# Kernel optimization log

Hardware: AMD Instinct MI355X
Metric: run time of the kernel (lower is better)

The kernel has to match this reference:

```python
import math
import jax, jax.numpy as jnp
import numpy as np

B, L, D_MODEL = 2, 2048, 768
H = 12            # num_heads == num_key_value_heads
FEAT = 16         # feature_dim
HEAD_DIM = D_MODEL // H  # 64


def taylor_exp(x):
    """Taylor-exp feature map: phi(x) = [1, x/rrd, (x (x) x)/(sqrt(2)*rd)].
    x: [..., d] -> [..., 1 + d + d^2]"""
    d = x.shape[-1]
    rd = math.sqrt(d)
    rrd = math.sqrt(rd)
    r2 = math.sqrt(2.0)
    x2 = (x[..., :, None] * x[..., None, :]).reshape(*x.shape[:-1], d * d) / r2
    ones = jnp.ones(x.shape[:-1] + (1,), dtype=x.dtype)
    return jnp.concatenate([ones, x / rrd, x2 / rd], axis=-1)


def setup_inputs() -> dict:
    key = jax.random.key(0)
    k1, k2, k3, k4, k5 = jax.random.split(key, 5)
    s = 0.02
    return {
        "hidden_states": jax.random.normal(k1, (B, L, D_MODEL), jnp.float32),
        "Wq": jax.random.normal(k2, (H * FEAT, D_MODEL), jnp.float32) * s,
        "Wk": jax.random.normal(k3, (H * FEAT, D_MODEL), jnp.float32) * s,
        "Wv": jax.random.normal(k4, (D_MODEL, D_MODEL), jnp.float32) * s,
        "Wo": jax.random.normal(k5, (D_MODEL, D_MODEL), jnp.float32) * s,
    }


def reference(hidden_states, Wq, Wk, Wv, Wo):
    b, l, d = hidden_states.shape
    # projections (torch Linear, no bias): y = x @ W.T
    q = jnp.einsum('bld,fd->blf', hidden_states, Wq).reshape(b, l, H, FEAT).transpose(0, 2, 1, 3)
    k = jnp.einsum('bld,fd->blf', hidden_states, Wk).reshape(b, l, H, FEAT).transpose(0, 2, 1, 3)
    v = jnp.einsum('bld,fd->blf', hidden_states, Wv).reshape(b, l, H, HEAD_DIM).transpose(0, 2, 1, 3)

    q = taylor_exp(q)   # [b,h,l,Dexp]
    k = taylor_exp(k)   # k_enc == k (forward clones k), v_enc == v

    # denominator: k_enc.sum over seq + causal cumsum of k
    k_state = jnp.sum(k, axis=2, keepdims=True) + jnp.cumsum(k, axis=2)  # [b,h,l,Dexp]
    z = 1.0 / jnp.sum(q * k_state, axis=-1)                              # [b,h,l]

    # quadratic scores; y1 uses causal (tril) mask, y2 uses full scores with same k,v
    A = jnp.einsum('bhnd,bhmd->bhnm', q, k)                              # [b,h,l,l]
    causal = jnp.tril(jnp.ones((l, l), dtype=A.dtype))
    A_total = A * causal + A                                             # tril(A) + A
    y = jnp.einsum('bhnm,bhme->bhne', A_total, v) * z[..., None]         # [b,h,l,e]

    out = y.transpose(0, 2, 1, 3).reshape(b, l, H * HEAD_DIM)
    return jnp.einsum('blf,df->bld', out, Wo)
```

## Files before the change

### kernel.cpp

```cpp
#include <hip/hip_runtime.h>

typedef unsigned short ushortT;
typedef __bf16 bf16x8 __attribute__((ext_vector_type(8)));
typedef float f32x4 __attribute__((ext_vector_type(4)));

#define BB   2
#define LL   2048
#define DM   768
#define HH   12
#define FT   16
#define HD   64
#define DEXP 273
#define CH   128
#define NC   16
#define NBH  24
#define NBLK 384
#define C2f  0.17677669529663687f
#define KH   768
#define KP   1536

__device__ __forceinline__ void split_bf16(float x, ushortT& hi, ushortT& lo) {
  unsigned b = __float_as_uint(x);
  unsigned r = b + 0x7FFFu + ((b >> 16) & 1u);
  hi = (ushortT)(r >> 16);
  float hf = __uint_as_float((unsigned)hi << 16);
  lo = (ushortT)(__float_as_uint(x - hf) >> 16);
}

__global__ __launch_bounds__(256) void pack_a(const float* __restrict__ X,
                                              ushortT* __restrict__ Xh,
                                              int total4) {
  int g = blockIdx.x * 256 + threadIdx.x;
  if (g >= total4) return;
  int m = g / 192, k4 = (g % 192) * 4;
  float4 v = *(const float4*)(X + (size_t)m * 768 + k4);
  ushortT h[4], l[4];
  split_bf16(v.x, h[0], l[0]);
  split_bf16(v.y, h[1], l[1]);
  split_bf16(v.z, h[2], l[2]);
  split_bf16(v.w, h[3], l[3]);
  ushortT* p = Xh + (size_t)m * KP + k4;
  *(ushort4*)p = *(ushort4*)h;
  *(ushort4*)(p + KH) = *(ushort4*)l;
}

__global__ __launch_bounds__(256) void pack_w(const float* __restrict__ W0,
                                              const float* __restrict__ W1,
                                              const float* __restrict__ W2,
                                              int n1, int n2,
                                              ushortT* __restrict__ Wh,
                                              int total4) {
  int g = blockIdx.x * 256 + threadIdx.x;
  if (g >= total4) return;
  int n = g / 192, k4 = (g % 192) * 4;
  const float* src = (n < n1 ? W0 + (size_t)n * 768
                    : n < n2 ? W1 + (size_t)(n - n1) * 768
                             : W2 + (size_t)(n - n2) * 768);
  float4 v = *(const float4*)(src + k4);
  ushortT h[4], l[4];
  split_bf16(v.x, h[0], l[0]);
  split_bf16(v.y, h[1], l[1]);
  split_bf16(v.z, h[2], l[2]);
  split_bf16(v.w, h[3], l[3]);
  ushortT* p = Wh + (size_t)n * KP + k4;
  *(ushort4*)p = *(ushort4*)h;
  *(ushort4*)(p + KH) = *(ushort4*)l;
}

typedef const __attribute__((address_space(1))) unsigned gq_t;
typedef __attribute__((address_space(3))) unsigned lq_t;
__device__ __forceinline__ void gload_lds16(const ushortT* g, ushortT* l) {
  __builtin_amdgcn_global_load_lds((gq_t*)g, (lq_t*)l, 16, 0, 0);
}

__global__ __launch_bounds__(256) void mfma_gemm(const ushortT* __restrict__ A,
                                                 const ushortT* __restrict__ B,
                                                 float* __restrict__ Y, int ldy,
                                                 int ntiles) {
  __shared__ ushortT sAh[128 * 32], sAl[128 * 32], sBh[64 * 32], sBl[64 * 32];
  const int blk = blockIdx.x;
  const int xcd = blk & 7, slot = blk >> 3;
  const int mtp = gridDim.x / (8 * ntiles);
  const int mt = xcd * mtp + slot / ntiles;
  const int nt = slot % ntiles;
  const int bm = mt * 128, bn = nt * 64;
  const int tid = threadIdx.x, wave = tid >> 6, lane = tid & 63;
  const int srow = lane >> 2, schk = (lane & 3) * 8;
  const ushortT* gsrc;
  ushortT* lb;
  int iters;
  switch (wave) {
    case 0:  gsrc = A + (size_t)(bm + srow) * KP + schk;      lb = sAh; iters = 8; break;
    case 1:  gsrc = A + (size_t)(bm + srow) * KP + KH + schk; lb = sAl; iters = 8; break;
    case 2:  gsrc = B + (size_t)(bn + srow) * KP + schk;      lb = sBh; iters = 4; break;
    default: gsrc = B + (size_t)(bn + srow) * KP + KH + schk; lb = sBl; iters = 4; break;
  }
  const int wm = (wave & 1) * 64, wn = (wave >> 1) * 32;
  const int fr = lane & 15, quad = lane >> 4;
  f32x4 acc[4][2] = {};
  for (int k0 = 0; k0 < KH; k0 += 32) {
    __syncthreads();
    for (int it = 0; it < iters; it++)
      gload_lds16(gsrc + k0 + (size_t)it * 16 * KP, lb + it * 512);
    __syncthreads();
    bf16x8 ah[4], al[4], bh2[2], bl2[2];
#pragma unroll
    for (int mi = 0; mi < 4; mi++) {
      ah[mi] = *(const bf16x8*)&sAh[(wm + mi * 16 + fr) * 32 + quad * 8];
      al[mi] = *(const bf16x8*)&sAl[(wm + mi * 16 + fr) * 32 + quad * 8];
    }
#pragma unroll
    for (int ni = 0; ni < 2; ni++) {
      bh2[ni] = *(const bf16x8*)&sBh[(wn + ni * 16 + fr) * 32 + quad * 8];
      bl2[ni] = *(const bf16x8*)&sBl[(wn + ni * 16 + fr) * 32 + quad * 8];
    }
#pragma unroll
    for (int mi = 0; mi < 4; mi++)
#pragma unroll
      for (int ni = 0; ni < 2; ni++) {
        acc[mi][ni] = __builtin_amdgcn_mfma_f32_16x16x32_bf16(ah[mi], bh2[ni], acc[mi][ni], 0, 0, 0);
        acc[mi][ni] = __builtin_amdgcn_mfma_f32_16x16x32_bf16(ah[mi], bl2[ni], acc[mi][ni], 0, 0, 0);
        acc[mi][ni] = __builtin_amdgcn_mfma_f32_16x16x32_bf16(al[mi], bh2[ni], acc[mi][ni], 0, 0, 0);
      }
  }
  const int orow = quad * 4;
#pragma unroll
  for (int mi = 0; mi < 4; mi++)
#pragma unroll
    for (int ni = 0; ni < 2; ni++) {
      float* yp = Y + (size_t)(bm + wm + mi * 16 + orow) * ldy + bn + wn + ni * 16 + fr;
#pragma unroll
      for (int r = 0; r < 4; r++) yp[(size_t)r * ldy] = acc[mi][ni][r];
    }
}

__global__ __launch_bounds__(256, 2) void chunk_sum_kernel(
    const float* __restrict__ qkv, float* __restrict__ csS,
    float* __restrict__ csk) {
  const int blk = blockIdx.x;
  const int bh = blk >> 4, c = blk & 15;
  const int b = bh / HH, h = bh % HH;
  __shared__ float kT[16][128];
  __shared__ ushortT phiA[288][72];
  __shared__ ushortT Vt[64][72];
  const float* base = qkv + (size_t)(b * LL + c * CH) * 1152;
  const int tid = threadIdx.x;
  const int wave = tid >> 6, lane = tid & 63;
  const int fr = lane & 15, quad = lane >> 4;
  for (int idx = tid; idx < 512; idx += 256) {
    int m = idx >> 2, i4 = (idx & 3) * 4;
    float4 k4 = *(const float4*)&base[(size_t)m * 1152 + 192 + h * 16 + i4];
    kT[i4 + 0][m] = k4.x; kT[i4 + 1][m] = k4.y;
    kT[i4 + 2][m] = k4.z; kT[i4 + 3][m] = k4.w;
  }
  const int wm2 = (wave & 1) * 144, wn2 = (wave >> 1) * 32;
  f32x4 acc[9][2] = {};
  __syncthreads();
#pragma unroll 1
  for (int s = 0; s < 4; s++) {
    const int m0 = s * 32;
    if (s) __syncthreads();
    for (int idx = tid; idx < 512; idx += 256) {
      int m = m0 + (idx >> 4), e4 = (idx & 15) * 4;
      float4 v4 = *(const float4*)&base[(size_t)m * 1152 + 384 + h * 64 + e4];
      ushortT hh[4], ll[4];
      split_bf16(v4.x, hh[0], ll[0]); split_bf16(v4.y, hh[1], ll[1]);
      split_bf16(v4.z, hh[2], ll[2]); split_bf16(v4.w, hh[3], ll[3]);
      const int mi2 = m - m0;
#pragma unroll
      for (int j = 0; j < 4; j++) {
        Vt[e4 + j][mi2] = hh[j];
        Vt[e4 + j][32 + mi2] = ll[j];
      }
    }
    for (int rr = tid; rr < 288; rr += 256) {
      const int f = rr;
      const float* pa = (f >= 17) ? kT[(f - 17) >> 4] : (f >= 1 ? kT[f - 1] : kT[0]);
      const float* pb = (f >= 17) ? kT[(f - 17) & 15] : kT[0];
      const float sc = (f == 0) ? 1.0f : (f < 17 ? 0.5f : C2f);
      const bool quadf = (f >= 17);
      const bool valid = (f < DEXP);
      ushortT hrow[32], lrow[32];
#pragma unroll
      for (int g = 0; g < 8; g++) {
        float4 a4 = *(const float4*)&pa[m0 + g * 4];
        float4 b4 = *(const float4*)&pb[m0 + g * 4];
        float v0, v1, v2, v3;
        if (f == 0) {
          v0 = v1 = v2 = v3 = 1.0f;
        } else if (!quadf) {
          v0 = sc * a4.x; v1 = sc * a4.y; v2 = sc * a4.z; v3 = sc * a4.w;
        } else {
          v0 = sc * a4.x * b4.x; v1 = sc * a4.y * b4.y;
          v2 = sc * a4.z * b4.z; v3 = sc * a4.w * b4.w;
        }
        if (!valid) { v0 = v1 = v2 = v3 = 0.0f; }
        split_bf16(v0, hrow[g * 4 + 0], lrow[g * 4 + 0]);
        split_bf16(v1, hrow[g * 4 + 1], lrow[g * 4 + 1]);
        split_bf16(v2, hrow[g * 4 + 2], lrow[g * 4 + 2]);
        split_bf16(v3, hrow[g * 4 + 3], lrow[g * 4 + 3]);
      }
      *(uint4*)&phiA[f][0] = *(uint4*)&hrow[0];
      *(uint4*)&phiA[f][8] = *(uint4*)&hrow[8];
      *(uint4*)&phiA[f][16] = *(uint4*)&hrow[16];
      *(uint4*)&phiA[f][24] = *(uint4*)&hrow[24];
      *(uint4*)&phiA[f][32] = *(uint4*)&lrow[0];
      *(uint4*)&phiA[f][40] = *(uint4*)&lrow[8];
      *(uint4*)&phiA[f][48] = *(uint4*)&lrow[16];
      *(uint4*)&phiA[f][56] = *(uint4*)&lrow[24];
    }
    __syncthreads();
    bf16x8 bhf[2], blf[2];
#pragma unroll
    for (int ni = 0; ni < 2; ni++) {
      bhf[ni] = *(const bf16x8*)&Vt[wn2 + ni * 16 + fr][quad * 8];
      blf[ni] = *(const bf16x8*)&Vt[wn2 + ni * 16 + fr][32 + quad * 8];
    }
#pragma unroll
    for (int mi = 0; mi < 9; mi++) {
      bf16x8 ah = *(const bf16x8*)&phiA[wm2 + mi * 16 + fr][quad * 8];
      bf16x8 al = *(const bf16x8*)&phiA[wm2 + mi * 16 + fr][32 + quad * 8];
#pragma unroll
      for (int ni = 0; ni < 2; ni++) {
        acc[mi][ni] = __builtin_amdgcn_mfma_f32_16x16x32_bf16(ah, bhf[ni], acc[mi][ni], 0, 0, 0);
        acc[mi][ni] = __builtin_amdgcn_mfma_f32_16x16x32_bf16(ah, blf[ni], acc[mi][ni], 0, 0, 0);
        acc[mi][ni] = __builtin_amdgcn_mfma_f32_16x16x32_bf16(al, bhf[ni], acc[mi][ni], 0, 0, 0);
      }
    }
  }
  for (int f = tid; f < DEXP; f += 256) {
    float sum = 0.0f;
    if (f == 0) {
      sum = (float)CH;
    } else if (f < 17) {
      const float* p = kT[f - 1];
      for (int m = 0; m < CH; m += 4) {
        float4 x = *(const float4*)&p[m];
        sum += x.x + x.y + x.z + x.w;
      }
      sum *= 0.5f;
    } else {
      const float* pa2 = kT[(f - 17) >> 4];
      const float* pb2 = kT[(f - 17) & 15];
      for (int m = 0; m < CH; m += 4) {
        float4 x = *(const float4*)&pa2[m];
        float4 y = *(const float4*)&pb2[m];
        sum += x.x * y.x + x.y * y.y + x.z * y.z + x.w * y.w;
      }
      sum *= C2f;
    }
    csk[(size_t)blk * DEXP + f] = sum;
  }
  float* S = csS + (size_t)blk * DEXP * 64;
#pragma unroll
  for (int mi = 0; mi < 9; mi++)
#pragma unroll
    for (int ni = 0; ni < 2; ni++)
#pragma unroll
      for (int r = 0; r < 4; r++) {
        const int f = wm2 + mi * 16 + quad * 4 + r;
        if (f < DEXP) S[(size_t)f * 64 + wn2 + ni * 16 + fr] = acc[mi][ni][r];
      }
}

__global__ __launch_bounds__(256) void prefix_kernel(float* __restrict__ csS,
                                                     float* __restrict__ csk) {
  const int gid = blockIdx.x * 256 + threadIdx.x;
  const int totS = NBH * DEXP * 64;
  if (gid < totS) {
    const int bh = gid / (DEXP * 64);
    const int idx = gid % (DEXP * 64);
    float r[NC];
    float tot = 0.0f;
#pragma unroll
    for (int c = 0; c < NC; c++) {
      r[c] = csS[(size_t)(bh * NC + c) * DEXP * 64 + idx];
      tot += r[c];
    }
    float run = 0.0f;
#pragma unroll
    for (int c = 0; c < NC; c++) {
      csS[(size_t)(bh * NC + c) * DEXP * 64 + idx] = run + tot;
      run += r[c];
    }
  } else {
    const int g2 = gid - totS;
    if (g2 < NBH * DEXP) {
      const int bh = g2 / DEXP;
      const int f = g2 % DEXP;
      float r[NC];
      float tot = 0.0f;
#pragma unroll
      for (int c = 0; c < NC; c++) {
        r[c] = csk[(size_t)(bh * NC + c) * DEXP + f];
        tot += r[c];
      }
      float run = 0.0f;
#pragma unroll
      for (int c = 0; c < NC; c++) {
        csk[(size_t)(bh * NC + c) * DEXP + f] = run + tot;
        run += r[c];
      }
    }
  }
}

__global__ __launch_bounds__(256, 2) void state_kernel(
    const float* __restrict__ qkv, const float* __restrict__ csS,
    float* __restrict__ att) {
  const int blk = blockIdx.x;
  const int bh = blk >> 4, c = blk & 15;
  const int b = bh / HH, h = bh % HH;
  __shared__ ushortT phiA[2][128][72];
  __shared__ ushortT Gt[2][64][72];
  const int tid = threadIdx.x;
  const int wv = tid >> 6, lane = tid & 63;
  const int prow = tid >> 1, phalf = tid & 1;
  const float* qrow = qkv + (size_t)(b * LL + c * CH + prow) * 1152 + h * 16;
  float qr[16];
#pragma unroll
  for (int i = 0; i < 4; i++) {
    float4 v = *(const float4*)(qrow + i * 4);
    qr[i * 4 + 0] = v.x; qr[i * 4 + 1] = v.y;
    qr[i * 4 + 2] = v.z; qr[i * 4 + 3] = v.w;
  }
  const float* Gc = csS + (size_t)blk * DEXP * 64;
  const int gfi = tid >> 4, gn4 = (tid & 15) * 4;

#define STAGE_SLAB(S, BB)                                                     \
  {                                                                           \
    const int f0 = (S) * 32;                                                  \
    _Pragma("unroll")                                                         \
    for (int p = 0; p < 2; p++) {                                             \
      const int fi = gfi + p * 16;                                            \
      const int f = f0 + fi;                                                  \
      float4 g = make_float4(0.f, 0.f, 0.f, 0.f);                             \
      if (f < DEXP) g = *(const float4*)(Gc + (size_t)f * 64 + gn4);          \
      ushortT gh[4], gl[4];                                                   \
      split_bf16(g.x, gh[0], gl[0]);                                          \
      split_bf16(g.y, gh[1], gl[1]);                                          \
      split_bf16(g.z, gh[2], gl[2]);                                          \
      split_bf16(g.w, gh[3], gl[3]);                                          \
      _Pragma("unroll")                                                       \
      for (int j = 0; j < 4; j++) {                                           \
        Gt[BB][gn4 + j][fi] = gh[j];                                          \
        Gt[BB][gn4 + j][32 + fi] = gl[j];                                     \
      }                                                                       \
    }                                                                         \
    ushortT h16[16], l16[16];                                                 \
    _Pragma("unroll")                                                         \
    for (int j = 0; j < 16; j++) {                                            \
      const int f = f0 + phalf * 16 + j;                                      \
      float v;                                                                \
      if (f == 0) v = 1.0f;                                                   \
      else if (f < 17) v = 0.5f * qr[f - 1];                                  \
      else if (f < DEXP) {                                                    \
        int ii = f - 17;                                                      \
        v = C2f * qr[ii >> 4] * qr[ii & 15];                                  \
      } else v = 0.0f;                                                        \
      split_bf16(v, h16[j], l16[j]);                                          \
    }                                                                         \
    *(uint4*)&phiA[BB][prow][phalf * 16] = *(uint4*)&h16[0];                  \
    *(uint4*)&phiA[BB][prow][phalf * 16 + 8] = *(uint4*)&h16[8];              \
    *(uint4*)&phiA[BB][prow][32 + phalf * 16] = *(uint4*)&l16[0];             \
    *(uint4*)&phiA[BB][prow][32 + phalf * 16 + 8] = *(uint4*)&l16[8];         \
  }

  const int fr = lane & 15, quad = lane >> 4;
  f32x4 acc[2][4] = {};
  STAGE_SLAB(0, 0);
  __syncthreads();
#pragma unroll 1
  for (int s = 0; s < 9; s++) {
    if (s < 8) STAGE_SLAB(s + 1, (s + 1) & 1);
    const int bb = s & 1;
    bf16x8 ah[2], al[2];
#pragma unroll
    for (int mi = 0; mi < 2; mi++) {
      ah[mi] = *(const bf16x8*)&phiA[bb][wv * 32 + mi * 16 + fr][quad * 8];
      al[mi] = *(const bf16x8*)&phiA[bb][wv * 32 + mi * 16 + fr][32 + quad * 8];
    }
#pragma unroll
    for (int ni = 0; ni < 4; ni++) {
      bf16x8 bh2 = *(const bf16x8*)&Gt[bb][ni * 16 + fr][quad * 8];
      bf16x8 bl2 = *(const bf16x8*)&Gt[bb][ni * 16 + fr][32 + quad * 8];
#pragma unroll
      for (int mi = 0; mi < 2; mi++) {
        acc[mi][ni] = __builtin_amdgcn_mfma_f32_16x16x32_bf16(ah[mi], bh2, acc[mi][ni], 0, 0, 0);
        acc[mi][ni] = __builtin_amdgcn_mfma_f32_16x16x32_bf16(ah[mi], bl2, acc[mi][ni], 0, 0, 0);
        acc[mi][ni] = __builtin_amdgcn_mfma_f32_16x16x32_bf16(al[mi], bh2, acc[mi][ni], 0, 0, 0);
      }
    }
    __syncthreads();
  }
  const int orow = quad * 4;
#pragma unroll
  for (int mi = 0; mi < 2; mi++)
#pragma unroll
    for (int ni = 0; ni < 4; ni++) {
      float* yp = att + (size_t)(b * LL + c * CH + wv * 32 + mi * 16 + orow) * DM +
                  h * 64 + ni * 16 + fr;
#pragma unroll
      for (int r = 0; r < 4; r++) yp[(size_t)r * DM] = acc[mi][ni][r];
    }
#undef STAGE_SLAB
}

__global__ __launch_bounds__(256) void intra_kernel(
    const float* __restrict__ qkv, const float* __restrict__ csk,
    float* __restrict__ att) {
  const int blk = blockIdx.x, tt = blockIdx.y;
  const int bh = blk >> 4, c = blk & 15;
  const int b = bh / HH, h = bh % HH;
  const int t0 = tt * 32, Mn = t0 + 32;
  __shared__ float ks[CH][17];
  __shared__ float vs[CH][68];
  __shared__ float qst[32][17];
  __shared__ float a_s[32][132];
  __shared__ float gkl[DEXP];
  __shared__ float dred[32][9];
  __shared__ float zl[32];
  const float* base = qkv + (size_t)(b * LL + c * CH) * 1152;
  const int tid = threadIdx.x;
  for (int idx = tid; idx < Mn * 16; idx += 256) {
    int m = idx >> 4, i = idx & 15;
    ks[m][i] = base[(size_t)m * 1152 + 192 + h * 16 + i];
  }
  for (int idx = tid; idx < Mn * 16; idx += 256) {
    int m = idx >> 4, e4g = (idx & 15) * 4;
    *(float4*)&vs[m][e4g] = *(const float4*)&base[(size_t)m * 1152 + 384 + h * 64 + e4g];
  }
  for (int idx = tid; idx < 32 * 16; idx += 256) {
    int t = idx >> 4, i = idx & 15;
    qst[t][i] = base[(size_t)(t0 + t) * 1152 + h * 16 + i];
  }
  for (int f = tid; f < DEXP; f += 256) gkl[f] = csk[(size_t)blk * DEXP + f];
  __syncthreads();
  for (int idx = tid; idx < 32 * CH; idx += 256) {
    const int t = idx >> 7, m = idx & 127;
    if (m < Mn) {
      float s = 0.0f;
#pragma unroll
      for (int i = 0; i < 16; i++) s += qst[t][i] * ks[m][i];
      a_s[t][m] = (m <= t0 + t) ? fmaf(s, fmaf(s, 0.03125f, 0.25f), 1.0f) : 0.0f;
    }
  }
  {
    const int t = tid >> 3, p = tid & 7;
    float part = (p == 0) ? gkl[0] : 0.0f;
#pragma unroll
    for (int ii = 0; ii < 2; ii++) {
      const int i = p * 2 + ii;
      const float qi = qst[t][i];
      part += 0.5f * qi * gkl[1 + i];
      float qsum = 0.0f;
#pragma unroll
      for (int j = 0; j < 16; j++) qsum += qst[t][j] * gkl[17 + i * 16 + j];
      part += C2f * qi * qsum;
    }
    dred[t][p] = part;
  }
  __syncthreads();
  if (tid < 32) {
    float dsum = 0.0f;
    for (int m = 0; m < Mn; m++) dsum += a_s[tid][m];
    float dstt = 0.0f;
#pragma unroll
    for (int p = 0; p < 8; p++) dstt += dred[tid][p];
    zl[tid] = 1.0f / (dstt + dsum);
  }
  __syncthreads();
  const int e4 = (tid & 15) * 4, tq = tid >> 4;
  float ac0[4] = {0, 0, 0, 0}, ac1[4] = {0, 0, 0, 0};
  for (int m = 0; m < Mn; m++) {
    float v4[4];
    *(float4*)v4 = *(const float4*)&vs[m][e4];
    const float a0 = a_s[tq][m], a1 = a_s[tq + 16][m];
#pragma unroll
    for (int j = 0; j < 4; j++) { ac0[j] += a0 * v4[j]; ac1[j] += a1 * v4[j]; }
  }
  const float z0 = zl[tq], z1 = zl[tq + 16];
  float* o0 = att + (size_t)(b * LL + c * CH + t0 + tq) * DM + h * 64 + e4;
  float* o1 = att + (size_t)(b * LL + c * CH + t0 + tq + 16) * DM + h * 64 + e4;
  float4 y0 = *(const float4*)o0;
  float4 y1 = *(const float4*)o1;
  float4 w0, w1;
  w0.x = (y0.x + ac0[0]) * z0; w0.y = (y0.y + ac0[1]) * z0;
  w0.z = (y0.z + ac0[2]) * z0; w0.w = (y0.w + ac0[3]) * z0;
  w1.x = (y1.x + ac1[0]) * z1; w1.y = (y1.y + ac1[1]) * z1;
  w1.z = (y1.z + ac1[2]) * z1; w1.w = (y1.w + ac1[3]) * z1;
  *(float4*)o0 = w0;
  *(float4*)o1 = w1;
}

extern "C" void kernel_launch(void* const* d_in, const int* in_sizes, int n_in,
                              void* d_out, int out_size, void* d_ws, size_t ws_size,
                              hipStream_t stream) {
  const float* hs = (const float*)d_in[0];
  const float* Wq = (const float*)d_in[1];
  const float* Wk = (const float*)d_in[2];
  const float* Wv = (const float*)d_in[3];
  const float* Wo = (const float*)d_in[4];
  float* out = (float*)d_out;
  char* ws = (char*)d_ws;
  float* qkv = (float*)(ws);
  float* att = (float*)(ws + 18874368);
  char*  regR = ws + 31457280;
  float* csS = (float*)regR;
  float* csk = (float*)(ws + 58294272);
  ushortT* Xhat = (ushortT*)regR;
  ushortT* What = (ushortT*)att;
  ushortT* Wohat = (ushortT*)qkv;
  ushortT* Ahat = (ushortT*)regR;
  const dim3 thr(256);
  pack_a<<<3072, thr, 0, stream>>>(hs, Xhat, 4096 * 192);
  pack_w<<<864, thr, 0, stream>>>(Wq, Wk, Wv, 192, 384, What, 1152 * 192);
  mfma_gemm<<<576, thr, 0, stream>>>(Xhat, What, qkv, 1152, 18);
  chunk_sum_kernel<<<NBLK, thr, 0, stream>>>(qkv, csS, csk);
  {
    const int tot = NBH * DEXP * 64 + NBH * DEXP;
    prefix_kernel<<<(tot + 255) / 256, thr, 0, stream>>>(csS, csk);
  }
  state_kernel<<<NBLK, thr, 0, stream>>>(qkv, csS, att);
  intra_kernel<<<dim3(NBLK, 4), thr, 0, stream>>>(qkv, csk, att);
  pack_w<<<576, thr, 0, stream>>>(Wo, Wo, Wo, 768, 768, Wohat, 768 * 192);
  pack_a<<<3072, thr, 0, stream>>>(att, Ahat, 4096 * 192);
  mfma_gemm<<<384, thr, 0, stream>>>(Ahat, Wohat, out, DM, 12);
}
```

Baseline: 273.5 us.

## Fuse state, intra-chunk attention and A packing into one MFMA kernel

Merges the inter-chunk state kernel, the intra-chunk scalar attention kernel and the pack_a of the attention output into a single kernel. The intra-chunk q·k scores and the P·V product now run on split-bf16 MFMA, and the row-sum denominator comes from an extra ones column. Normalised output is written straight in the hi/lo packed layout the output GEMM expects. This removes two launches, the att round trip through global memory and the scalar intra loop. In exchange the double buffering in the state loop is dropped, and the extra shared memory and registers may lower occupancy.

```diff
diff --git a/kernel.cpp b/kernel.cpp
--- a/kernel.cpp
+++ b/kernel.cpp
@@ -305,18 +305,26 @@
   }
 }
 
-__global__ __launch_bounds__(256, 2) void state_kernel(
+__global__ __launch_bounds__(256, 2) void fused_out(
     const float* __restrict__ qkv, const float* __restrict__ csS,
-    float* __restrict__ att) {
+    const float* __restrict__ csk, ushortT* __restrict__ Ahat) {
   const int blk = blockIdx.x;
   const int bh = blk >> 4, c = blk & 15;
   const int b = bh / HH, h = bh % HH;
-  __shared__ ushortT phiA[2][128][72];
-  __shared__ ushortT Gt[2][64][72];
+  __shared__ ushortT phiA[128][72];
+  __shared__ ushortT Gt[64][72];
+  __shared__ ushortT qA1[128][40];
+  __shared__ ushortT qA2[128][40];
+  __shared__ ushortT kB[32][40];
+  __shared__ ushortT onesB[16][72];
+  __shared__ float dred[128][2];
+  __shared__ float zl[128];
   const int tid = threadIdx.x;
   const int wv = tid >> 6, lane = tid & 63;
+  const int fr = lane & 15, quad = lane >> 4;
   const int prow = tid >> 1, phalf = tid & 1;
-  const float* qrow = qkv + (size_t)(b * LL + c * CH + prow) * 1152 + h * 16;
+  const float* base = qkv + (size_t)(b * LL + c * CH) * 1152;
+  const float* qrow = base + (size_t)prow * 1152 + h * 16;
   float qr[16];
 #pragma unroll
   for (int i = 0; i < 4; i++) {
@@ -324,66 +332,75 @@
     qr[i * 4 + 0] = v.x; qr[i * 4 + 1] = v.y;
     qr[i * 4 + 2] = v.z; qr[i * 4 + 3] = v.w;
   }
+  {
+    ushortT qh[16], ql[16];
+#pragma unroll
+    for (int i = 0; i < 16; i++) split_bf16(qr[i], qh[i], ql[i]);
+    *(uint4*)&qA1[prow][phalf * 16] = *(uint4*)&qh[0];
+    *(uint4*)&qA1[prow][phalf * 16 + 8] = *(uint4*)&qh[8];
+    *(uint4*)&qA2[prow][phalf * 16] = *(uint4*)&ql[0];
+    *(uint4*)&qA2[prow][phalf * 16 + 8] = *(uint4*)&ql[8];
+  }
+  for (int idx = tid; idx < 16 * 64; idx += 256) {
+    int row = idx >> 6, k = idx & 63;
+    onesB[row][k] = (row == 0 && k < 32) ? (ushortT)0x3F80 : (ushortT)0;
+  }
   const float* Gc = csS + (size_t)blk * DEXP * 64;
+  const float* gkp = csk + (size_t)blk * DEXP;
   const int gfi = tid >> 4, gn4 = (tid & 15) * 4;
-
-#define STAGE_SLAB(S, BB)                                                     \
-  {                                                                           \
-    const int f0 = (S) * 32;                                                  \
-    _Pragma("unroll")                                                         \
-    for (int p = 0; p < 2; p++) {                                             \
-      const int fi = gfi + p * 16;                                            \
-      const int f = f0 + fi;                                                  \
-      float4 g = make_float4(0.f, 0.f, 0.f, 0.f);                             \
-      if (f < DEXP) g = *(const float4*)(Gc + (size_t)f * 64 + gn4);          \
-      ushortT gh[4], gl[4];                                                   \
-      split_bf16(g.x, gh[0], gl[0]);                                          \
-      split_bf16(g.y, gh[1], gl[1]);                                          \
-      split_bf16(g.z, gh[2], gl[2]);                                          \
-      split_bf16(g.w, gh[3], gl[3]);                                          \
-      _Pragma("unroll")                                                       \
-      for (int j = 0; j < 4; j++) {                                           \
-        Gt[BB][gn4 + j][fi] = gh[j];                                          \
-        Gt[BB][gn4 + j][32 + fi] = gl[j];                                     \
-      }                                                                       \
-    }                                                                         \
-    ushortT h16[16], l16[16];                                                 \
-    _Pragma("unroll")                                                         \
-    for (int j = 0; j < 16; j++) {                                            \
-      const int f = f0 + phalf * 16 + j;                                      \
-      float v;                                                                \
-      if (f == 0) v = 1.0f;                                                   \
-      else if (f < 17) v = 0.5f * qr[f - 1];                                  \
-      else if (f < DEXP) {                                                    \
-        int ii = f - 17;                                                      \
-        v = C2f * qr[ii >> 4] * qr[ii & 15];                                  \
-      } else v = 0.0f;                                                        \
-      split_bf16(v, h16[j], l16[j]);                                          \
-    }                                                                         \
-    *(uint4*)&phiA[BB][prow][phalf * 16] = *(uint4*)&h16[0];                  \
-    *(uint4*)&phiA[BB][prow][phalf * 16 + 8] = *(uint4*)&h16[8];              \
-    *(uint4*)&phiA[BB][prow][32 + phalf * 16] = *(uint4*)&l16[0];             \
-    *(uint4*)&phiA[BB][prow][32 + phalf * 16 + 8] = *(uint4*)&l16[8];         \
-  }
-
-  const int fr = lane & 15, quad = lane >> 4;
-  f32x4 acc[2][4] = {};
-  STAGE_SLAB(0, 0);
-  __syncthreads();
+  f32x4 acc[2][5] = {};
+  float dacc = 0.0f;
 #pragma unroll 1
   for (int s = 0; s < 9; s++) {
-    if (s < 8) STAGE_SLAB(s + 1, (s + 1) & 1);
-    const int bb = s & 1;
+    const int f0 = s * 32;
+#pragma unroll
+    for (int p = 0; p < 2; p++) {
+      const int fi = gfi + p * 16;
+      const int f = f0 + fi;
+      float4 g = make_float4(0.f, 0.f, 0.f, 0.f);
+      if (f < DEXP) g = *(const float4*)(Gc + (size_t)f * 64 + gn4);
+      ushortT gh[4], gl[4];
+      split_bf16(g.x, gh[0], gl[0]);
+      split_bf16(g.y, gh[1], gl[1]);
+      split_bf16(g.z, gh[2], gl[2]);
+      split_bf16(g.w, gh[3], gl[3]);
+#pragma unroll
+      for (int j = 0; j < 4; j++) {
+        Gt[gn4 + j][fi] = gh[j];
+        Gt[gn4 + j][32 + fi] = gl[j];
+      }
+    }
+    {
+      ushortT h16[16], l16[16];
+#pragma unroll
+      for (int j = 0; j < 16; j++) {
+        const int f = f0 + phalf * 16 + j;
+        float v;
+        if (f == 0) v = 1.0f;
+        else if (f < 17) v = 0.5f * qr[f - 1];
+        else if (f < DEXP) {
+          int ii = f - 17;
+          v = C2f * qr[ii >> 4] * qr[ii & 15];
+        } else v = 0.0f;
+        if (f < DEXP) dacc += v * gkp[f];
+        split_bf16(v, h16[j], l16[j]);
+      }
+      *(uint4*)&phiA[prow][phalf * 16] = *(uint4*)&h16[0];
+      *(uint4*)&phiA[prow][phalf * 16 + 8] = *(uint4*)&h16[8];
+      *(uint4*)&phiA[prow][32 + phalf * 16] = *(uint4*)&l16[0];
+      *(uint4*)&phiA[prow][32 + phalf * 16 + 8] = *(uint4*)&l16[8];
+    }
+    __syncthreads();
     bf16x8 ah[2], al[2];
 #pragma unroll
     for (int mi = 0; mi < 2; mi++) {
-      ah[mi] = *(const bf16x8*)&phiA[bb][wv * 32 + mi * 16 + fr][quad * 8];
-      al[mi] = *(const bf16x8*)&phiA[bb][wv * 32 + mi * 16 + fr][32 + quad * 8];
+      ah[mi] = *(const bf16x8*)&phiA[wv * 32 + mi * 16 + fr][quad * 8];
+      al[mi] = *(const bf16x8*)&phiA[wv * 32 + mi * 16 + fr][32 + quad * 8];
     }
 #pragma unroll
     for (int ni = 0; ni < 4; ni++) {
-      bf16x8 bh2 = *(const bf16x8*)&Gt[bb][ni * 16 + fr][quad * 8];
-      bf16x8 bl2 = *(const bf16x8*)&Gt[bb][ni * 16 + fr][32 + quad * 8];
+      bf16x8 bh2 = *(const bf16x8*)&Gt[ni * 16 + fr][quad * 8];
+      bf16x8 bl2 = *(const bf16x8*)&Gt[ni * 16 + fr][32 + quad * 8];
 #pragma unroll
       for (int mi = 0; mi < 2; mi++) {
         acc[mi][ni] = __builtin_amdgcn_mfma_f32_16x16x32_bf16(ah[mi], bh2, acc[mi][ni], 0, 0, 0);
@@ -393,104 +410,100 @@
     }
     __syncthreads();
   }
-  const int orow = quad * 4;
+  dred[prow][phalf] = dacc;
+#pragma unroll 1
+  for (int s = 0; s < 4; s++) {
+    const int m0 = s * 32;
+    for (int idx = tid; idx < 128; idx += 256) {
+      int mL = idx >> 2, i4 = (idx & 3) * 4;
+      float4 k4 = *(const float4*)&base[(size_t)(m0 + mL) * 1152 + 192 + h * 16 + i4];
+      ushortT hh[4], ll[4];
+      split_bf16(k4.x, hh[0], ll[0]); split_bf16(k4.y, hh[1], ll[1]);
+      split_bf16(k4.z, hh[2], ll[2]); split_bf16(k4.w, hh[3], ll[3]);
+      *(ushort4*)&kB[mL][i4] = *(ushort4*)hh;
+      *(ushort4*)&kB[mL][16 + i4] = *(ushort4*)ll;
+    }
+    for (int idx = tid; idx < 512; idx += 256) {
+      int mL = idx >> 4, e4 = (idx & 15) * 4;
+      float4 v4 = *(const float4*)&base[(size_t)(m0 + mL) * 1152 + 384 + h * 64 + e4];
+      ushortT hh[4], ll[4];
+      split_bf16(v4.x, hh[0], ll[0]); split_bf16(v4.y, hh[1], ll[1]);
+      split_bf16(v4.z, hh[2], ll[2]); split_bf16(v4.w, hh[3], ll[3]);
+#pragma unroll
+      for (int j = 0; j < 4; j++) {
+        Gt[e4 + j][mL] = hh[j];
+        Gt[e4 + j][32 + mL] = ll[j];
+      }
+    }
+    __syncthreads();
+    if (s <= wv) {
+#pragma unroll
+      for (int rt = 0; rt < 2; rt++) {
+        bf16x8 a1 = *(const bf16x8*)&qA1[wv * 32 + rt * 16 + fr][quad * 8];
+        bf16x8 a2 = *(const bf16x8*)&qA2[wv * 32 + rt * 16 + fr][quad * 8];
+#pragma unroll
+        for (int mtt = 0; mtt < 2; mtt++) {
+          bf16x8 bk = *(const bf16x8*)&kB[mtt * 16 + fr][quad * 8];
+          f32x4 sf = {};
+          sf = __builtin_amdgcn_mfma_f32_16x16x32_bf16(a1, bk, sf, 0, 0, 0);
+          sf = __builtin_amdgcn_mfma_f32_16x16x32_bf16(a2, bk, sf, 0, 0, 0);
+          const int mg = m0 + mtt * 16 + fr;
+#pragma unroll
+          for (int r = 0; r < 4; r++) {
+            const int rowL = wv * 32 + rt * 16 + quad * 4 + r;
+            const float sv = sf[r];
+            const float p = (mg <= rowL) ? fmaf(sv, fmaf(sv, 0.03125f, 0.25f), 1.0f) : 0.0f;
+            ushortT ph, pl;
+            split_bf16(p, ph, pl);
+            phiA[rowL][mtt * 16 + fr] = ph;
+            phiA[rowL][32 + mtt * 16 + fr] = pl;
+          }
+        }
+      }
+#pragma unroll
+      for (int mi = 0; mi < 2; mi++) {
+        bf16x8 ah = *(const bf16x8*)&phiA[wv * 32 + mi * 16 + fr][quad * 8];
+        bf16x8 al = *(const bf16x8*)&phiA[wv * 32 + mi * 16 + fr][32 + quad * 8];
+#pragma unroll
+        for (int ni = 0; ni < 5; ni++) {
+          bf16x8 bh2 = (ni < 4) ? *(const bf16x8*)&Gt[ni * 16 + fr][quad * 8]
+                                : *(const bf16x8*)&onesB[fr][quad * 8];
+          bf16x8 bl2 = (ni < 4) ? *(const bf16x8*)&Gt[ni * 16 + fr][32 + quad * 8]
+                                : *(const bf16x8*)&onesB[fr][32 + quad * 8];
+          acc[mi][ni] = __builtin_amdgcn_mfma_f32_16x16x32_bf16(ah, bh2, acc[mi][ni], 0, 0, 0);
+          acc[mi][ni] = __builtin_amdgcn_mfma_f32_16x16x32_bf16(ah, bl2, acc[mi][ni], 0, 0, 0);
+          acc[mi][ni] = __builtin_amdgcn_mfma_f32_16x16x32_bf16(al, bh2, acc[mi][ni], 0, 0, 0);
+        }
+      }
+    }
+    __syncthreads();
+  }
+  if (fr == 0) {
+#pragma unroll
+    for (int mi = 0; mi < 2; mi++)
+#pragma unroll
+      for (int r = 0; r < 4; r++) {
+        const int rowL = wv * 32 + mi * 16 + quad * 4 + r;
+        const float d = dred[rowL][0] + dred[rowL][1] + acc[mi][4][r];
+        zl[rowL] = 1.0f / d;
+      }
+  }
+  __syncthreads();
+  const size_t rowbase = (size_t)(b * LL + c * CH);
 #pragma unroll
   for (int mi = 0; mi < 2; mi++)
 #pragma unroll
-    for (int ni = 0; ni < 4; ni++) {
-      float* yp = att + (size_t)(b * LL + c * CH + wv * 32 + mi * 16 + orow) * DM +
-                  h * 64 + ni * 16 + fr;
-#pragma unroll
-      for (int r = 0; r < 4; r++) yp[(size_t)r * DM] = acc[mi][ni][r];
-    }
-#undef STAGE_SLAB
-}
-
-__global__ __launch_bounds__(256) void intra_kernel(
-    const float* __restrict__ qkv, const float* __restrict__ csk,
-    float* __restrict__ att) {
-  const int blk = blockIdx.x, tt = blockIdx.y;
-  const int bh = blk >> 4, c = blk & 15;
-  const int b = bh / HH, h = bh % HH;
-  const int t0 = tt * 32, Mn = t0 + 32;
-  __shared__ float ks[CH][17];
-  __shared__ float vs[CH][68];
-  __shared__ float qst[32][17];
-  __shared__ float a_s[32][132];
-  __shared__ float gkl[DEXP];
-  __shared__ float dred[32][9];
-  __shared__ float zl[32];
-  const float* base = qkv + (size_t)(b * LL + c * CH) * 1152;
-  const int tid = threadIdx.x;
-  for (int idx = tid; idx < Mn * 16; idx += 256) {
-    int m = idx >> 4, i = idx & 15;
-    ks[m][i] = base[(size_t)m * 1152 + 192 + h * 16 + i];
-  }
-  for (int idx = tid; idx < Mn * 16; idx += 256) {
-    int m = idx >> 4, e4g = (idx & 15) * 4;
-    *(float4*)&vs[m][e4g] = *(const float4*)&base[(size_t)m * 1152 + 384 + h * 64 + e4g];
-  }
-  for (int idx = tid; idx < 32 * 16; idx += 256) {
-    int t = idx >> 4, i = idx & 15;
-    qst[t][i] = base[(size_t)(t0 + t) * 1152 + h * 16 + i];
-  }
-  for (int f = tid; f < DEXP; f += 256) gkl[f] = csk[(size_t)blk * DEXP + f];
-  __syncthreads();
-  for (int idx = tid; idx < 32 * CH; idx += 256) {
-    const int t = idx >> 7, m = idx & 127;
-    if (m < Mn) {
-      float s = 0.0f;
-#pragma unroll
-      for (int i = 0; i < 16; i++) s += qst[t][i] * ks[m][i];
-      a_s[t][m] = (m <= t0 + t) ? fmaf(s, fmaf(s, 0.03125f, 0.25f), 1.0f) : 0.0f;
-    }
-  }
-  {
-    const int t = tid >> 3, p = tid & 7;
-    float part = (p == 0) ? gkl[0] : 0.0f;
-#pragma unroll
-    for (int ii = 0; ii < 2; ii++) {
-      const int i = p * 2 + ii;
-      const float qi = qst[t][i];
-      part += 0.5f * qi * gkl[1 + i];
-      float qsum = 0.0f;
-#pragma unroll
-      for (int j = 0; j < 16; j++) qsum += qst[t][j] * gkl[17 + i * 16 + j];
-      part += C2f * qi * qsum;
-    }
-    dred[t][p] = part;
-  }
-  __syncthreads();
-  if (tid < 32) {
-    float dsum = 0.0f;
-    for (int m = 0; m < Mn; m++) dsum += a_s[tid][m];
-    float dstt = 0.0f;
-#pragma unroll
-    for (int p = 0; p < 8; p++) dstt += dred[tid][p];
-    zl[tid] = 1.0f / (dstt + dsum);
-  }
-  __syncthreads();
-  const int e4 = (tid & 15) * 4, tq = tid >> 4;
-  float ac0[4] = {0, 0, 0, 0}, ac1[4] = {0, 0, 0, 0};
-  for (int m = 0; m < Mn; m++) {
-    float v4[4];
-    *(float4*)v4 = *(const float4*)&vs[m][e4];
-    const float a0 = a_s[tq][m], a1 = a_s[tq + 16][m];
-#pragma unroll
-    for (int j = 0; j < 4; j++) { ac0[j] += a0 * v4[j]; ac1[j] += a1 * v4[j]; }
-  }
-  const float z0 = zl[tq], z1 = zl[tq + 16];
-  float* o0 = att + (size_t)(b * LL + c * CH + t0 + tq) * DM + h * 64 + e4;
-  float* o1 = att + (size_t)(b * LL + c * CH + t0 + tq + 16) * DM + h * 64 + e4;
-  float4 y0 = *(const float4*)o0;
-  float4 y1 = *(const float4*)o1;
-  float4 w0, w1;
-  w0.x = (y0.x + ac0[0]) * z0; w0.y = (y0.y + ac0[1]) * z0;
-  w0.z = (y0.z + ac0[2]) * z0; w0.w = (y0.w + ac0[3]) * z0;
-  w1.x = (y1.x + ac1[0]) * z1; w1.y = (y1.y + ac1[1]) * z1;
-  w1.z = (y1.z + ac1[2]) * z1; w1.w = (y1.w + ac1[3]) * z1;
-  *(float4*)o0 = w0;
-  *(float4*)o1 = w1;
+    for (int ni = 0; ni < 4; ni++)
+#pragma unroll
+      for (int r = 0; r < 4; r++) {
+        const int rowL = wv * 32 + mi * 16 + quad * 4 + r;
+        const float val = acc[mi][ni][r] * zl[rowL];
+        ushortT hh, ll;
+        split_bf16(val, hh, ll);
+        ushortT* ap = Ahat + (rowbase + rowL) * (size_t)KP + h * 64 + ni * 16 + fr;
+        ap[0] = hh;
+        ap[KH] = ll;
+      }
 }
 
 extern "C" void kernel_launch(void* const* d_in, const int* in_sizes, int n_in,
@@ -504,14 +517,14 @@
   float* out = (float*)d_out;
   char* ws = (char*)d_ws;
   float* qkv = (float*)(ws);
-  float* att = (float*)(ws + 18874368);
+  char*  attR = ws + 18874368;
   char*  regR = ws + 31457280;
   float* csS = (float*)regR;
   float* csk = (float*)(ws + 58294272);
   ushortT* Xhat = (ushortT*)regR;
-  ushortT* What = (ushortT*)att;
+  ushortT* What = (ushortT*)attR;
+  ushortT* Ahat = (ushortT*)attR;
   ushortT* Wohat = (ushortT*)qkv;
-  ushortT* Ahat = (ushortT*)regR;
   const dim3 thr(256);
   pack_a<<<3072, thr, 0, stream>>>(hs, Xhat, 4096 * 192);
   pack_w<<<864, thr, 0, stream>>>(Wq, Wk, Wv, 192, 384, What, 1152 * 192);
@@ -521,9 +534,7 @@
     const int tot = NBH * DEXP * 64 + NBH * DEXP;
     prefix_kernel<<<(tot + 255) / 256, thr, 0, stream>>>(csS, csk);
   }
-  state_kernel<<<NBLK, thr, 0, stream>>>(qkv, csS, att);
-  intra_kernel<<<dim3(NBLK, 4), thr, 0, stream>>>(qkv, csk, att);
+  fused_out<<<NBLK, thr, 0, stream>>>(qkv, csS, csk, Ahat);
   pack_w<<<576, thr, 0, stream>>>(Wo, Wo, Wo, 768, 768, Wohat, 768 * 192);
-  pack_a<<<3072, thr, 0, stream>>>(att, Ahat, 4096 * 192);
   mfma_gemm<<<384, thr, 0, stream>>>(Ahat, Wohat, out, DM, 12);
 }
```

Measured after the change: 262.9 us. 1.04x faster.
